# Kernel optimization log

Measured on AMD Instinct MI355X. Metric: run time of the kernel, lower is better.

The kernel has to match this reference:

```python
import jax, jax.numpy as jnp
import numpy as np

EMBED_DIM = 384
NUM_HEADS = 6
HEAD_DIM = EMBED_DIM // NUM_HEADS
MLP_HIDDEN = 4 * EMBED_DIM
LN_EPS = 1e-5


def layer_norm(x, gamma, beta):
    mu = jnp.mean(x, axis=-1, keepdims=True)
    var = jnp.mean((x - mu) ** 2, axis=-1, keepdims=True)
    return (x - mu) * jax.lax.rsqrt(var + LN_EPS) * gamma + beta


def setup_inputs() -> dict:
    key = jax.random.key(0)
    ks = jax.random.split(key, 8)
    D, H = EMBED_DIM, MLP_HIDDEN
    s = 1.0 / np.sqrt(D)
    sh = 1.0 / np.sqrt(H)
    return {
        "x": jax.random.normal(ks[0], (16, 1024, D), dtype=jnp.float32),
        "ln1_g": jnp.ones((D,), jnp.float32),
        "ln1_b": jnp.zeros((D,), jnp.float32),
        "qkv_w": jax.random.uniform(ks[1], (3 * D, D), jnp.float32, -s, s),
        "qkv_b": jax.random.uniform(ks[2], (3 * D,), jnp.float32, -s, s),
        "proj_w": jax.random.uniform(ks[3], (D, D), jnp.float32, -s, s),
        "proj_b": jax.random.uniform(ks[4], (D,), jnp.float32, -s, s),
        "ln2_g": jnp.ones((D,), jnp.float32),
        "ln2_b": jnp.zeros((D,), jnp.float32),
        "fc1_w": jax.random.uniform(ks[5], (H, D), jnp.float32, -s, s),
        "fc1_b": jax.random.uniform(ks[6], (H,), jnp.float32, -s, s),
        "fc2_w": jax.random.uniform(ks[7], (D, H), jnp.float32, -sh, sh),
        "fc2_b": jnp.zeros((D,), jnp.float32),
    }


def reference(x, ln1_g, ln1_b, qkv_w, qkv_b, proj_w, proj_b,
              ln2_g, ln2_b, fc1_w, fc1_b, fc2_w, fc2_b):
    B, N, D = x.shape
    Hh, Dh = NUM_HEADS, HEAD_DIM
    scale = Dh ** -0.5

    # --- attention sublayer (pre-norm) ---
    h = layer_norm(x, ln1_g, ln1_b)
    qkv = h @ qkv_w.T + qkv_b                      # [B,N,3D]
    qkv = qkv.reshape(B, N, 3, Hh, Dh)
    q, k, v = (qkv[:, :, i].transpose(0, 2, 1, 3) for i in range(3))  # [B,H,N,Dh]
    attn = jax.nn.softmax(jnp.einsum('bhnd,bhmd->bhnm', q, k) * scale, axis=-1)
    o = jnp.einsum('bhnm,bhmd->bhnd', attn, v)     # [B,H,N,Dh]
    o = o.transpose(0, 2, 1, 3).reshape(B, N, D)
    x = x + (o @ proj_w.T + proj_b)

    # --- MLP sublayer (pre-norm) ---
    h = layer_norm(x, ln2_g, ln2_b)
    h = jax.nn.gelu(h @ fc1_w.T + fc1_b, approximate=False)
    x = x + (h @ fc2_w.T + fc2_b)
    return x
```

## Files before the change

### kernel.cpp

```cpp
#include <hip/hip_runtime.h>

typedef unsigned short u16;
typedef unsigned int   u32;
typedef __bf16  bf16x8 __attribute__((ext_vector_type(8)));
typedef __bf16  bf16x4_t __attribute__((ext_vector_type(4)));
typedef float   f32x4  __attribute__((ext_vector_type(4)));

struct Ptrs { const void* p[13]; };

extern "C" __device__ float __ocml_native_exp2_f32(float);

__device__ __forceinline__ float bf2f(u16 u) {
    union { unsigned int i; float f; } c; c.i = ((unsigned int)u) << 16; return c.f;
}
__device__ __forceinline__ u16 f2bf(float f) {
    union { float f; unsigned int i; } c; c.f = f;
    unsigned int u = c.i;
    unsigned int r = (u + 0x7fffu + ((u >> 16) & 1u)) >> 16;
    return (u16)r;
}

__device__ __forceinline__ float wave_sum(float x) {
#pragma unroll
    for (int m = 32; m >= 1; m >>= 1) x += __shfl_xor(x, m);
    return x;
}

__device__ __forceinline__ void g2l16(const u16* g, u16* l) {
    __builtin_amdgcn_global_load_lds(
        (__attribute__((address_space(1))) void*)g,
        (__attribute__((address_space(3))) void*)l, 16, 0, 0);
}

__global__ void k_flag(const u32* __restrict__ w, int* __restrict__ flagp)
{
    if (threadIdx.x == 0) {
        int cnt = 0;
        for (int i = 0; i < 128; ++i) {
            u16 lo = (u16)(w[i] & 0xFFFFu);
            int e = (lo >> 7) & 0xFF;
            cnt += (e >= 117 && e <= 123) ? 1 : 0;
        }
        *flagp = (cnt >= 64) ? 1 : 0;
    }
}

__global__ __launch_bounds__(256) void k_convert(Ptrs ps,
                                                 u16* __restrict__ cw,
                                                 const int* __restrict__ flagp)
{
    const int cum[13] = {0,48,96,55392,55536,73968,74016,74064,74112,
                         147840,148032,221760,221808};
    const int off[12] = {0,384,768,443136,444288,591744,
                         592128,592512,592896,1182720,1184256,1774080};
    int c = blockIdx.x * 256 + threadIdx.x;
    if (c >= 221808) return;
    int seg = 0;
#pragma unroll
    for (int i = 1; i < 12; ++i) seg += (c >= cum[i]) ? 1 : 0;
    int e = (c - cum[seg]) * 8;
    u16* dst = cw + off[seg] + e;
    if (*flagp) {
        *(uint4*)dst = *((const uint4*)ps.p[seg + 1] + (e >> 3));
    } else {
        const float* s = (const float*)ps.p[seg + 1] + e;
        u16 tmp[8];
#pragma unroll
        for (int t = 0; t < 8; ++t) tmp[t] = f2bf(s[t]);
        *(uint4*)dst = *(const uint4*)tmp;
    }
}

__global__ __launch_bounds__(256) void k_ln1cvt(const void* __restrict__ xin,
                                                const u16* __restrict__ g,
                                                const u16* __restrict__ b,
                                                u16* __restrict__ cx,
                                                u16* __restrict__ h,
                                                const int* __restrict__ flagp)
{
    const int wid = threadIdx.x >> 6, lane = threadIdx.x & 63;
    const int row = blockIdx.x * 4 + wid;
    float v[6]; u16 raw[6];
    if (*flagp) {
        const u16* p = (const u16*)xin + (size_t)row * 384;
#pragma unroll
        for (int t = 0; t < 6; t++) { raw[t] = p[lane + 64 * t]; v[t] = bf2f(raw[t]); }
    } else {
        const float* p = (const float*)xin + (size_t)row * 384;
#pragma unroll
        for (int t = 0; t < 6; t++) { v[t] = p[lane + 64 * t]; raw[t] = f2bf(v[t]); }
    }
    u16* pc = cx + (size_t)row * 384;
#pragma unroll
    for (int t = 0; t < 6; t++) pc[lane + 64 * t] = raw[t];
    float s = 0.f;
#pragma unroll
    for (int t = 0; t < 6; t++) s += v[t];
    const float mu = wave_sum(s) * (1.0f / 384.0f);
    float vs = 0.f;
#pragma unroll
    for (int t = 0; t < 6; t++) { float d = v[t] - mu; vs += d * d; }
    const float var = wave_sum(vs) * (1.0f / 384.0f);
    const float rs = rsqrtf(var + 1e-5f);
    u16* po = h + (size_t)row * 384;
#pragma unroll
    for (int t = 0; t < 6; t++) {
        int e = lane + 64 * t;
        po[e] = f2bf((v[t] - mu) * rs * bf2f(g[e]) + bf2f(b[e]));
    }
}

__device__ __forceinline__ void gemm_core_128(const u16* __restrict__ A,
                                              const u16* __restrict__ B,
                                              int K, int m0, int n0,
                                              f32x4 (&acc)[4][4])
{
    __shared__ __align__(16) u16 As[128 * 64];
    __shared__ __align__(16) u16 Bs[128 * 64];

    const int tid  = threadIdx.x;
    const int lane = tid & 63;
    const int wid  = tid >> 6;
    const int wm  = (wid >> 1) * 64;
    const int wn  = (wid & 1) * 64;
    const int l15 = lane & 15;
    const int g   = lane >> 4;
    const int srow   = lane >> 3;
    const int schunk = ((lane & 7) ^ srow) * 8;

    const u16* Abase = A + (size_t)(m0 + wid * 32 + srow) * K + schunk;
    const u16* Bbase = B + (size_t)(n0 + wid * 32 + srow) * K + schunk;

    for (int kk = 0; kk < K; kk += 64) {
        __syncthreads();
#pragma unroll
        for (int t = 0; t < 4; ++t) {
            g2l16(Abase + (size_t)t * 8 * K + kk, &As[(wid * 32 + t * 8) * 64]);
            g2l16(Bbase + (size_t)t * 8 * K + kk, &Bs[(wid * 32 + t * 8) * 64]);
        }
        __syncthreads();

#pragma unroll
        for (int ks = 0; ks < 2; ++ks) {
            bf16x8 af[4], bfr[4];
#pragma unroll
            for (int i = 0; i < 4; i++) {
                int row = wm + 16 * i + l15;
                int p = ((ks * 4 + g) ^ (l15 & 7)) * 8;
                af[i] = __builtin_bit_cast(bf16x8,
                         *(const uint4*)&As[row * 64 + p]);
            }
#pragma unroll
            for (int j = 0; j < 4; j++) {
                int row = wn + 16 * j + l15;
                int p = ((ks * 4 + g) ^ (l15 & 7)) * 8;
                bfr[j] = __builtin_bit_cast(bf16x8,
                         *(const uint4*)&Bs[row * 64 + p]);
            }
#pragma unroll
            for (int i = 0; i < 4; i++)
#pragma unroll
                for (int j = 0; j < 4; j++)
                    acc[i][j] = __builtin_amdgcn_mfma_f32_16x16x32_bf16(
                                    af[i], bfr[j], acc[i][j], 0, 0, 0);
        }
    }
}

__device__ __forceinline__ void gemm_core_128x64(const u16* __restrict__ A,
                                                 const u16* __restrict__ B,
                                                 int K, int m0, int n0,
                                                 f32x4 (&acc)[4][2])
{
    __shared__ __align__(16) u16 As[128 * 64];
    __shared__ __align__(16) u16 Bs[64 * 64];

    const int tid  = threadIdx.x;
    const int lane = tid & 63;
    const int wid  = tid >> 6;
    const int wm  = (wid >> 1) * 64;
    const int wn  = (wid & 1) * 32;
    const int l15 = lane & 15;
    const int g   = lane >> 4;
    const int srow   = lane >> 3;
    const int schunk = ((lane & 7) ^ srow) * 8;

    const u16* Abase = A + (size_t)(m0 + wid * 32 + srow) * K + schunk;
    const u16* Bbase = B + (size_t)(n0 + wid * 16 + srow) * K + schunk;

    for (int kk = 0; kk < K; kk += 64) {
        __syncthreads();
#pragma unroll
        for (int t = 0; t < 4; ++t)
            g2l16(Abase + (size_t)t * 8 * K + kk, &As[(wid * 32 + t * 8) * 64]);
#pragma unroll
        for (int t = 0; t < 2; ++t)
            g2l16(Bbase + (size_t)t * 8 * K + kk, &Bs[(wid * 16 + t * 8) * 64]);
        __syncthreads();

#pragma unroll
        for (int ks = 0; ks < 2; ++ks) {
            bf16x8 af[4], bfr[2];
#pragma unroll
            for (int i = 0; i < 4; i++) {
                int row = wm + 16 * i + l15;
                int p = ((ks * 4 + g) ^ (l15 & 7)) * 8;
                af[i] = __builtin_bit_cast(bf16x8,
                         *(const uint4*)&As[row * 64 + p]);
            }
#pragma unroll
            for (int j = 0; j < 2; j++) {
                int row = wn + 16 * j + l15;
                int p = ((ks * 4 + g) ^ (l15 & 7)) * 8;
                bfr[j] = __builtin_bit_cast(bf16x8,
                         *(const uint4*)&Bs[row * 64 + p]);
            }
#pragma unroll
            for (int i = 0; i < 4; i++)
#pragma unroll
                for (int j = 0; j < 2; j++)
                    acc[i][j] = __builtin_amdgcn_mfma_f32_16x16x32_bf16(
                                    af[i], bfr[j], acc[i][j], 0, 0, 0);
        }
    }
}

__global__ __launch_bounds__(256) void k_layernorm(const u16* __restrict__ in,
                                                   const u16* __restrict__ g,
                                                   const u16* __restrict__ b,
                                                   u16* __restrict__ out,
                                                   int nrows)
{
    const int wid = threadIdx.x >> 6, lane = threadIdx.x & 63;
    const int row = blockIdx.x * 4 + wid;
    if (row >= nrows) return;
    float v[6];
    const u16* p = in + (size_t)row * 384;
#pragma unroll
    for (int t = 0; t < 6; t++) v[t] = bf2f(p[lane + 64 * t]);
    float s = 0.f;
#pragma unroll
    for (int t = 0; t < 6; t++) s += v[t];
    const float mu = wave_sum(s) * (1.0f / 384.0f);
    float vs = 0.f;
#pragma unroll
    for (int t = 0; t < 6; t++) { float d = v[t] - mu; vs += d * d; }
    const float var = wave_sum(vs) * (1.0f / 384.0f);
    const float rs = rsqrtf(var + 1e-5f);
    u16* po = out + (size_t)row * 384;
#pragma unroll
    for (int t = 0; t < 6; t++) {
        int e = lane + 64 * t;
        po[e] = f2bf((v[t] - mu) * rs * bf2f(g[e]) + bf2f(b[e]));
    }
}

__global__ __launch_bounds__(256) void k_gemm_qkv(const u16* __restrict__ A,
                                                  const u16* __restrict__ W,
                                                  const u16* __restrict__ bias,
                                                  u16* __restrict__ q,
                                                  u16* __restrict__ k,
                                                  u16* __restrict__ vrow)
{
    const int id = blockIdx.x, slot = id & 7, idx = id >> 3;
    const int m0 = (slot * 16 + idx / 9) * 128;
    const int n0 = (idx % 9) * 128;
    f32x4 acc[4][4];
#pragma unroll
    for (int i = 0; i < 4; i++)
#pragma unroll
        for (int j = 0; j < 4; j++) acc[i][j] = f32x4{0.f, 0.f, 0.f, 0.f};
    gemm_core_128(A, W, 384, m0, n0, acc);
    const int lane = threadIdx.x & 63, wid = threadIdx.x >> 6;
    const int wm = (wid >> 1) * 64, wn = (wid & 1) * 64;
    const int l15 = lane & 15, rq = (lane >> 4) * 4;
#pragma unroll
    for (int i = 0; i < 4; i++)
#pragma unroll
        for (int j = 0; j < 4; j++)
#pragma unroll
            for (int r = 0; r < 4; r++) {
                int gr = m0 + wm + 16 * i + rq + r;
                int gc = n0 + wn + 16 * j + l15;
                float v = acc[i][j][r] + bf2f(bias[gc]);
                int part = gc / 384, rem = gc % 384;
                int head = rem >> 6, dh = rem & 63;
                int bb = gr >> 10, nn = gr & 1023;
                int bh = bb * 6 + head;
                u16* dst = (part == 0) ? q : (part == 1) ? k : vrow;
                dst[((size_t)bh * 1024 + nn) * 64 + dh] = f2bf(v);
            }
}

__global__ __launch_bounds__(256) void k_transpose_v(const u16* __restrict__ v,
                                                     u16* __restrict__ vT)
{
    __shared__ u16 T[64 * 72];
    const int bh = blockIdx.y, n0 = blockIdx.x * 64;
    const int tid = threadIdx.x;
    const int r = tid >> 2;
    const int c = (tid & 3) * 16;
    const u16* src = v + (size_t)bh * 65536 + (size_t)(n0 + r) * 64 + c;
    uint4 a = *(const uint4*)src;
    uint4 b = *(const uint4*)(src + 8);
    u16 buf[16];
    *(uint4*)&buf[0] = a; *(uint4*)&buf[8] = b;
#pragma unroll
    for (int e = 0; e < 16; ++e) T[(c + e) * 72 + r] = buf[e];
    __syncthreads();
    uint4 o0 = *(const uint4*)&T[r * 72 + c];
    uint4 o1 = *(const uint4*)&T[r * 72 + c + 8];
    u16* dst = vT + (size_t)bh * 65536 + (size_t)r * 1024 + n0 + c;
    *(uint4*)dst = o0;
    *(uint4*)(dst + 8) = o1;
}

__global__ __launch_bounds__(256) void k_attn(const u16* __restrict__ q,
                                              const u16* __restrict__ kk,
                                              const u16* __restrict__ vT,
                                              u16* __restrict__ o)
{
    __shared__ __align__(16) u16 Ks[128 * 64];
    __shared__ __align__(16) u16 Vs[2][64 * 64];
    __shared__ __align__(16) u16 Ps[128 * 64];

    const int tid = threadIdx.x, lane = tid & 63, wid = tid >> 6;
    const int l15 = lane & 15, g = lane >> 4, q8 = g * 8;
    const int id = blockIdx.x;
    const int bh = (id & 7) * 12 + ((id >> 3) >> 3);
    const int q0 = ((id >> 3) & 7) * 128;
    const int wrow = wid * 32;

    const u16* Q = q  + (size_t)bh * 65536;
    const u16* K = kk + (size_t)bh * 65536;
    const u16* V = vT + (size_t)bh * 65536;

    const int srow   = lane >> 3;
    const int schunk = ((lane & 7) ^ srow) * 8;
    const int rd0 = ((0 + g) ^ (l15 & 7)) * 8;
    const int rd1 = ((4 + g) ^ (l15 & 7)) * 8;
    int pcol[4];
#pragma unroll
    for (int ip = 0; ip < 4; ++ip)
        pcol[ip] = (((ip * 2 + (g >> 1)) ^ (l15 & 7)) * 8) + (g & 1) * 4;

    bf16x8 aq[2][2];
#pragma unroll
    for (int jp = 0; jp < 2; ++jp)
#pragma unroll
        for (int ks = 0; ks < 2; ++ks) {
            bf16x8 t = __builtin_bit_cast(bf16x8,
                *(const uint4*)&Q[(size_t)(q0 + wrow + jp * 16 + l15) * 64
                                  + ks * 32 + q8]);
#pragma unroll
            for (int e = 0; e < 8; ++e)
                t[e] = (__bf16)((float)t[e] * 0.18033688f);
            aq[jp][ks] = t;
        }

    f32x4 ob[2][4];
#pragma unroll
    for (int i = 0; i < 2; ++i)
#pragma unroll
        for (int j = 0; j < 4; ++j) ob[i][j] = f32x4{0.f, 0.f, 0.f, 0.f};
    float lsum[2] = {0.f, 0.f};

    for (int kt2 = 0; kt2 < 8; ++kt2) {
        __syncthreads();
#pragma unroll
        for (int t = 0; t < 4; ++t) {
            int r0 = wid * 32 + t * 8;
            g2l16(&K[(size_t)(kt2 * 128 + r0 + srow) * 64 + schunk], &Ks[r0 * 64]);
        }
#pragma unroll
        for (int h = 0; h < 2; ++h)
#pragma unroll
            for (int t = 0; t < 2; ++t) {
                int r0 = wid * 16 + t * 8;
                g2l16(&V[(size_t)(r0 + srow) * 1024 + kt2 * 128 + h * 64 + schunk],
                      &Vs[h][r0 * 64]);
            }
        __syncthreads();

#pragma unroll 1
        for (int h = 0; h < 2; ++h) {
            f32x4 st[4][2];
#pragma unroll
            for (int ip = 0; ip < 4; ++ip)
#pragma unroll
                for (int jp = 0; jp < 2; ++jp) st[ip][jp] = f32x4{0.f,0.f,0.f,0.f};
#pragma unroll
            for (int ip = 0; ip < 4; ++ip) {
                int rbase = (h * 64 + ip * 16 + l15) * 64;
                bf16x8 bk0 = __builtin_bit_cast(bf16x8,
                    *(const uint4*)&Ks[rbase + rd0]);
                bf16x8 bk1 = __builtin_bit_cast(bf16x8,
                    *(const uint4*)&Ks[rbase + rd1]);
#pragma unroll
                for (int jp = 0; jp < 2; ++jp) {
                    st[ip][jp] = __builtin_amdgcn_mfma_f32_16x16x32_bf16(
                                    bk0, aq[jp][0], st[ip][jp], 0, 0, 0);
                    st[ip][jp] = __builtin_amdgcn_mfma_f32_16x16x32_bf16(
                                    bk1, aq[jp][1], st[ip][jp], 0, 0, 0);
                }
            }

#pragma unroll
            for (int jp = 0; jp < 2; ++jp) {
                float ps = 0.f;
#pragma unroll
                for (int ip = 0; ip < 4; ++ip)
#pragma unroll
                    for (int r = 0; r < 4; ++r) {
                        float p = __ocml_native_exp2_f32(st[ip][jp][r]);
                        st[ip][jp][r] = p;
                        ps += p;
                    }
                lsum[jp] += ps;
            }

#pragma unroll
            for (int ip = 0; ip < 4; ++ip)
#pragma unroll
                for (int jp = 0; jp < 2; ++jp) {
                    bf16x4_t pk;
#pragma unroll
                    for (int r = 0; r < 4; ++r) pk[r] = (__bf16)st[ip][jp][r];
                    *(bf16x4_t*)&Ps[(wrow + jp*16 + l15) * 64 + pcol[ip]] = pk;
                }

#pragma unroll
            for (int ks = 0; ks < 2; ++ks) {
                const int rdo = ks ? rd1 : rd0;
                bf16x8 ap[2];
#pragma unroll
                for (int i = 0; i < 2; ++i)
                    ap[i] = __builtin_bit_cast(bf16x8,
                        *(const uint4*)&Ps[(wrow + i*16 + l15) * 64 + rdo]);
#pragma unroll
                for (int jv = 0; jv < 4; ++jv) {
                    bf16x8 bv = __builtin_bit_cast(bf16x8,
                        *(const uint4*)&Vs[h][(jv * 16 + l15) * 64 + rdo]);
#pragma unroll
                    for (int i = 0; i < 2; ++i)
                        ob[i][jv] = __builtin_amdgcn_mfma_f32_16x16x32_bf16(
                                      ap[i], bv, ob[i][jv], 0, 0, 0);
                }
            }
        }
    }

#pragma unroll
    for (int jp = 0; jp < 2; ++jp) {
        lsum[jp] += __shfl_xor(lsum[jp], 16);
        lsum[jp] += __shfl_xor(lsum[jp], 32);
    }
    const int bb = bh / 6, hh = bh % 6;
#pragma unroll
    for (int i = 0; i < 2; ++i)
#pragma unroll
        for (int r = 0; r < 4; ++r) {
            int src = (lane & 48) | (g * 4 + r);
            float linv = 1.0f / __shfl(lsum[i], src);
            int row = q0 + wrow + i * 16 + g * 4 + r;
#pragma unroll
            for (int jv = 0; jv < 4; ++jv) {
                int dh = jv * 16 + l15;
                o[((size_t)(bb * 1024 + row)) * 384 + hh * 64 + dh] =
                    f2bf(ob[i][jv][r] * linv);
            }
        }
}

__global__ __launch_bounds__(256) void k_gemm_proj(const u16* __restrict__ A,
                                                   const u16* __restrict__ W,
                                                   const u16* __restrict__ bias,
                                                   const u16* __restrict__ xin,
                                                   u16* __restrict__ x1)
{
    const int id = blockIdx.x, slot = id & 7, idx = id >> 3;
    const int m0 = (slot * 16 + idx / 6) * 128;
    const int n0 = (idx % 6) * 64;
    f32x4 acc[4][2];
#pragma unroll
    for (int i = 0; i < 4; i++)
#pragma unroll
        for (int j = 0; j < 2; j++) acc[i][j] = f32x4{0.f, 0.f, 0.f, 0.f};
    gemm_core_128x64(A, W, 384, m0, n0, acc);
    const int lane = threadIdx.x & 63, wid = threadIdx.x >> 6;
    const int wm = (wid >> 1) * 64, wn = (wid & 1) * 32;
    const int l15 = lane & 15, rq = (lane >> 4) * 4;
#pragma unroll
    for (int i = 0; i < 4; i++)
#pragma unroll
        for (int j = 0; j < 2; j++)
#pragma unroll
            for (int r = 0; r < 4; r++) {
                int gr = m0 + wm + 16 * i + rq + r;
                int gc = n0 + wn + 16 * j + l15;
                size_t ix = (size_t)gr * 384 + gc;
                x1[ix] = f2bf(acc[i][j][r] + bf2f(bias[gc]) + bf2f(xin[ix]));
            }
}

__global__ __launch_bounds__(256) void k_gemm_fc1(const u16* __restrict__ A,
                                                  const u16* __restrict__ W,
                                                  const u16* __restrict__ bias,
                                                  u16* __restrict__ hmid)
{
    const int id = blockIdx.x, slot = id & 7, idx = id >> 3;
    const int mbase = (slot * 8 + idx / 12) * 256;
    const int n0 = (idx % 12) * 128;
#pragma unroll 1
    for (int sub = 0; sub < 2; ++sub) {
        const int m0 = mbase + sub * 128;
        f32x4 acc[4][4];
#pragma unroll
        for (int i = 0; i < 4; i++)
#pragma unroll
            for (int j = 0; j < 4; j++) acc[i][j] = f32x4{0.f, 0.f, 0.f, 0.f};
        gemm_core_128(A, W, 384, m0, n0, acc);
        const int lane = threadIdx.x & 63, wid = threadIdx.x >> 6;
        const int wm = (wid >> 1) * 64, wn = (wid & 1) * 64;
        const int l15 = lane & 15, rq = (lane >> 4) * 4;
#pragma unroll
        for (int i = 0; i < 4; i++)
#pragma unroll
            for (int j = 0; j < 4; j++)
#pragma unroll
                for (int r = 0; r < 4; r++) {
                    int gr = m0 + wm + 16 * i + rq + r;
                    int gc = n0 + wn + 16 * j + l15;
                    float v = acc[i][j][r] + bf2f(bias[gc]);
                    float u = v * (1.5957691f + 0.0713548f * v * v);
                    float ge = v * __builtin_amdgcn_rcpf(1.0f + __expf(-u));
                    hmid[(size_t)gr * 1536 + gc] = f2bf(ge);
                }
    }
}

__global__ __launch_bounds__(256) void k_gemm_fc2(const u16* __restrict__ A,
                                                  const u16* __restrict__ W,
                                                  const u16* __restrict__ bias,
                                                  const u16* __restrict__ x1,
                                                  void* __restrict__ outv,
                                                  const int* __restrict__ flagp)
{
    const int id = blockIdx.x, slot = id & 7, idx = id >> 3;
    const int m0 = (slot * 16 + idx / 6) * 128;
    const int n0 = (idx % 6) * 64;
    f32x4 acc[4][2];
#pragma unroll
    for (int i = 0; i < 4; i++)
#pragma unroll
        for (int j = 0; j < 2; j++) acc[i][j] = f32x4{0.f, 0.f, 0.f, 0.f};
    gemm_core_128x64(A, W, 1536, m0, n0, acc);
    const int lane = threadIdx.x & 63, wid = threadIdx.x >> 6;
    const int wm = (wid >> 1) * 64, wn = (wid & 1) * 32;
    const int l15 = lane & 15, rq = (lane >> 4) * 4;
    const int isbf = *flagp;
    u16*   ob = (u16*)outv;
    float* of = (float*)outv;
#pragma unroll
    for (int i = 0; i < 4; i++)
#pragma unroll
        for (int j = 0; j < 2; j++)
#pragma unroll
            for (int r = 0; r < 4; r++) {
                int gr = m0 + wm + 16 * i + rq + r;
                int gc = n0 + wn + 16 * j + l15;
                size_t ix = (size_t)gr * 384 + gc;
                float v = acc[i][j][r] + bf2f(bias[gc]) + bf2f(x1[ix]);
                if (isbf) ob[ix] = f2bf(v);
                else      of[ix] = v;
            }
}

extern "C" void kernel_launch(void* const* d_in, const int* in_sizes, int n_in,
                              void* d_out, int out_size, void* d_ws, size_t ws_size,
                              hipStream_t stream)
{
    char* ws = (char*)d_ws;
    u16*   cw   = (u16*)(ws + 0);
    int*   flag = (int*)(ws + 3548928);
    u16*   cx   = (u16*)(ws + 3549184);
    u16*   h    = (u16*)(ws + 16132096);
    u16*   x1   = (u16*)(ws + 28715008);
    u16*   q    = (u16*)(ws + 53880832);
    u16*   kbuf = (u16*)(ws + 66463744);
    u16*   vT   = (u16*)(ws + 79046656);
    u16*   o    = (u16*)(ws + 91629568);
    u16*   vrow = o;
    u16*   hmid = (u16*)(ws + 53880832);

    const u16* c_ln1_g  = cw + 0;
    const u16* c_ln1_b  = cw + 384;
    const u16* c_qkv_w  = cw + 768;
    const u16* c_qkv_b  = cw + 443136;
    const u16* c_proj_w = cw + 444288;
    const u16* c_proj_b = cw + 591744;
    const u16* c_ln2_g  = cw + 592128;
    const u16* c_ln2_b  = cw + 592512;
    const u16* c_fc1_w  = cw + 592896;
    const u16* c_fc1_b  = cw + 1182720;
    const u16* c_fc2_w  = cw + 1184256;
    const u16* c_fc2_b  = cw + 1774080;

    Ptrs ps;
    for (int i = 0; i < 13; ++i) ps.p[i] = d_in[i];

    k_flag<<<1, 64, 0, stream>>>((const u32*)d_in[3], flag);
    k_convert<<<867, 256, 0, stream>>>(ps, cw, flag);
    k_ln1cvt<<<4096, 256, 0, stream>>>(d_in[0], c_ln1_g, c_ln1_b, cx, h, flag);
    k_gemm_qkv<<<1152, 256, 0, stream>>>(h, c_qkv_w, c_qkv_b, q, kbuf, vrow);
    k_transpose_v<<<dim3(16, 96), 256, 0, stream>>>(vrow, vT);
    k_attn<<<768, 256, 0, stream>>>(q, kbuf, vT, o);
    k_gemm_proj<<<768, 256, 0, stream>>>(o, c_proj_w, c_proj_b, cx, x1);
    k_layernorm<<<4096, 256, 0, stream>>>(x1, c_ln2_g, c_ln2_b, h, 16384);
    k_gemm_fc1<<<768, 256, 0, stream>>>(h, c_fc1_w, c_fc1_b, hmid);
    k_gemm_fc2<<<768, 256, 0, stream>>>(hmid, c_fc2_w, c_fc2_b, x1,
                                        d_out, flag);
    (void)in_sizes; (void)n_in; (void)out_size; (void)ws_size; (void)c_fc2_b;
}
```

Measured before the change: 271.7 us.

## Double-buffer K in LDS, load V directly to registers, vectorize layernorm

The attention kernel now prefetches the next K tile into registers while the current tile is computed, writes it into a second LDS buffer, and needs only one barrier per iteration. V fragments are read straight from global memory into registers instead of being staged through LDS. The MFMA sections are wrapped in s_setprio hints. The layernorm kernels switch to contiguous per-lane 6-element chunks with 32-bit and 64-bit loads and stores. This trades higher register pressure and uncoalesced direct V loads from global for fewer LDS round-trips and barriers.

```diff
diff --git a/kernel.cpp b/kernel.cpp
--- a/kernel.cpp
+++ b/kernel.cpp
@@ -5,6 +5,7 @@
 typedef __bf16  bf16x8 __attribute__((ext_vector_type(8)));
 typedef __bf16  bf16x4_t __attribute__((ext_vector_type(4)));
 typedef float   f32x4  __attribute__((ext_vector_type(4)));
+typedef float   f32x2  __attribute__((ext_vector_type(2)));
 
 struct Ptrs { const void* p[13]; };
 
@@ -80,19 +81,32 @@
 {
     const int wid = threadIdx.x >> 6, lane = threadIdx.x & 63;
     const int row = blockIdx.x * 4 + wid;
+    const int e0 = lane * 6;
     float v[6]; u16 raw[6];
     if (*flagp) {
-        const u16* p = (const u16*)xin + (size_t)row * 384;
-#pragma unroll
-        for (int t = 0; t < 6; t++) { raw[t] = p[lane + 64 * t]; v[t] = bf2f(raw[t]); }
+        const u16* p = (const u16*)xin + (size_t)row * 384 + e0;
+        u32 w0 = *(const u32*)(p);
+        u32 w1 = *(const u32*)(p + 2);
+        u32 w2 = *(const u32*)(p + 4);
+        raw[0] = (u16)w0; raw[1] = (u16)(w0 >> 16);
+        raw[2] = (u16)w1; raw[3] = (u16)(w1 >> 16);
+        raw[4] = (u16)w2; raw[5] = (u16)(w2 >> 16);
+#pragma unroll
+        for (int t = 0; t < 6; t++) v[t] = bf2f(raw[t]);
     } else {
-        const float* p = (const float*)xin + (size_t)row * 384;
-#pragma unroll
-        for (int t = 0; t < 6; t++) { v[t] = p[lane + 64 * t]; raw[t] = f2bf(v[t]); }
-    }
-    u16* pc = cx + (size_t)row * 384;
-#pragma unroll
-    for (int t = 0; t < 6; t++) pc[lane + 64 * t] = raw[t];
+        const float* p = (const float*)xin + (size_t)row * 384 + e0;
+        f32x2 a0 = *(const f32x2*)(p);
+        f32x2 a1 = *(const f32x2*)(p + 2);
+        f32x2 a2 = *(const f32x2*)(p + 4);
+        v[0] = a0[0]; v[1] = a0[1]; v[2] = a1[0];
+        v[3] = a1[1]; v[4] = a2[0]; v[5] = a2[1];
+#pragma unroll
+        for (int t = 0; t < 6; t++) raw[t] = f2bf(v[t]);
+    }
+    u32* pc = (u32*)(cx + (size_t)row * 384 + e0);
+    pc[0] = (u32)raw[0] | ((u32)raw[1] << 16);
+    pc[1] = (u32)raw[2] | ((u32)raw[3] << 16);
+    pc[2] = (u32)raw[4] | ((u32)raw[5] << 16);
     float s = 0.f;
 #pragma unroll
     for (int t = 0; t < 6; t++) s += v[t];
@@ -102,12 +116,21 @@
     for (int t = 0; t < 6; t++) { float d = v[t] - mu; vs += d * d; }
     const float var = wave_sum(vs) * (1.0f / 384.0f);
     const float rs = rsqrtf(var + 1e-5f);
-    u16* po = h + (size_t)row * 384;
+    const u32* gg = (const u32*)(g + e0);
+    const u32* bb = (const u32*)(b + e0);
+    u32 gw[3] = {gg[0], gg[1], gg[2]};
+    u32 bw[3] = {bb[0], bb[1], bb[2]};
+    u16 ow[6];
 #pragma unroll
     for (int t = 0; t < 6; t++) {
-        int e = lane + 64 * t;
-        po[e] = f2bf((v[t] - mu) * rs * bf2f(g[e]) + bf2f(b[e]));
-    }
+        u16 ge = (u16)(gw[t >> 1] >> ((t & 1) * 16));
+        u16 be = (u16)(bw[t >> 1] >> ((t & 1) * 16));
+        ow[t] = f2bf((v[t] - mu) * rs * bf2f(ge) + bf2f(be));
+    }
+    u32* po = (u32*)(h + (size_t)row * 384 + e0);
+    po[0] = (u32)ow[0] | ((u32)ow[1] << 16);
+    po[1] = (u32)ow[2] | ((u32)ow[3] << 16);
+    po[2] = (u32)ow[4] | ((u32)ow[5] << 16);
 }
 
 __device__ __forceinline__ void gemm_core_128(const u16* __restrict__ A,
@@ -234,10 +257,15 @@
     const int wid = threadIdx.x >> 6, lane = threadIdx.x & 63;
     const int row = blockIdx.x * 4 + wid;
     if (row >= nrows) return;
+    const int e0 = lane * 6;
     float v[6];
-    const u16* p = in + (size_t)row * 384;
-#pragma unroll
-    for (int t = 0; t < 6; t++) v[t] = bf2f(p[lane + 64 * t]);
+    const u16* p = in + (size_t)row * 384 + e0;
+    u32 w0 = *(const u32*)(p);
+    u32 w1 = *(const u32*)(p + 2);
+    u32 w2 = *(const u32*)(p + 4);
+    v[0] = bf2f((u16)w0); v[1] = bf2f((u16)(w0 >> 16));
+    v[2] = bf2f((u16)w1); v[3] = bf2f((u16)(w1 >> 16));
+    v[4] = bf2f((u16)w2); v[5] = bf2f((u16)(w2 >> 16));
     float s = 0.f;
 #pragma unroll
     for (int t = 0; t < 6; t++) s += v[t];
@@ -247,12 +275,21 @@
     for (int t = 0; t < 6; t++) { float d = v[t] - mu; vs += d * d; }
     const float var = wave_sum(vs) * (1.0f / 384.0f);
     const float rs = rsqrtf(var + 1e-5f);
-    u16* po = out + (size_t)row * 384;
+    const u32* gg = (const u32*)(g + e0);
+    const u32* bb = (const u32*)(b + e0);
+    u32 gw[3] = {gg[0], gg[1], gg[2]};
+    u32 bw[3] = {bb[0], bb[1], bb[2]};
+    u16 ow[6];
 #pragma unroll
     for (int t = 0; t < 6; t++) {
-        int e = lane + 64 * t;
-        po[e] = f2bf((v[t] - mu) * rs * bf2f(g[e]) + bf2f(b[e]));
-    }
+        u16 ge = (u16)(gw[t >> 1] >> ((t & 1) * 16));
+        u16 be = (u16)(bw[t >> 1] >> ((t & 1) * 16));
+        ow[t] = f2bf((v[t] - mu) * rs * bf2f(ge) + bf2f(be));
+    }
+    u32* po = (u32*)(out + (size_t)row * 384 + e0);
+    po[0] = (u32)ow[0] | ((u32)ow[1] << 16);
+    po[1] = (u32)ow[2] | ((u32)ow[3] << 16);
+    po[2] = (u32)ow[4] | ((u32)ow[5] << 16);
 }
 
 __global__ __launch_bounds__(256) void k_gemm_qkv(const u16* __restrict__ A,
@@ -320,8 +357,7 @@
                                               const u16* __restrict__ vT,
                                               u16* __restrict__ o)
 {
-    __shared__ __align__(16) u16 Ks[128 * 64];
-    __shared__ __align__(16) u16 Vs[2][64 * 64];
+    __shared__ __align__(16) u16 Ks[2][128 * 64];
     __shared__ __align__(16) u16 Ps[128 * 64];
 
     const int tid = threadIdx.x, lane = tid & 63, wid = tid >> 6;
@@ -358,6 +394,15 @@
             aq[jp][ks] = t;
         }
 
+    uint4 kreg[4];
+#pragma unroll
+    for (int t = 0; t < 4; ++t)
+        kreg[t] = *(const uint4*)&K[(size_t)(wid * 32 + t * 8 + srow) * 64 + schunk];
+#pragma unroll
+    for (int t = 0; t < 4; ++t)
+        *(uint4*)&Ks[0][(wid * 32 + t * 8) * 64 + lane * 8] = kreg[t];
+    __syncthreads();
+
     f32x4 ob[2][4];
 #pragma unroll
     for (int i = 0; i < 2; ++i)
@@ -365,37 +410,41 @@
         for (int j = 0; j < 4; ++j) ob[i][j] = f32x4{0.f, 0.f, 0.f, 0.f};
     float lsum[2] = {0.f, 0.f};
 
+    int cur = 0;
     for (int kt2 = 0; kt2 < 8; ++kt2) {
-        __syncthreads();
-#pragma unroll
-        for (int t = 0; t < 4; ++t) {
-            int r0 = wid * 32 + t * 8;
-            g2l16(&K[(size_t)(kt2 * 128 + r0 + srow) * 64 + schunk], &Ks[r0 * 64]);
-        }
-#pragma unroll
-        for (int h = 0; h < 2; ++h)
-#pragma unroll
-            for (int t = 0; t < 2; ++t) {
-                int r0 = wid * 16 + t * 8;
-                g2l16(&V[(size_t)(r0 + srow) * 1024 + kt2 * 128 + h * 64 + schunk],
-                      &Vs[h][r0 * 64]);
-            }
-        __syncthreads();
+        if (kt2 < 7) {
+#pragma unroll
+            for (int t = 0; t < 4; ++t)
+                kreg[t] = *(const uint4*)
+                    &K[(size_t)((kt2 + 1) * 128 + wid * 32 + t * 8 + srow) * 64
+                       + schunk];
+        }
 
 #pragma unroll 1
         for (int h = 0; h < 2; ++h) {
+            uint4 vreg[2][4];
+#pragma unroll
+            for (int ks = 0; ks < 2; ++ks)
+#pragma unroll
+                for (int jv = 0; jv < 4; ++jv)
+                    vreg[ks][jv] = *(const uint4*)
+                        &V[(size_t)(jv * 16 + l15) * 1024
+                           + kt2 * 128 + h * 64 + (ks * 4 + g) * 8];
+
             f32x4 st[4][2];
 #pragma unroll
             for (int ip = 0; ip < 4; ++ip)
 #pragma unroll
                 for (int jp = 0; jp < 2; ++jp) st[ip][jp] = f32x4{0.f,0.f,0.f,0.f};
+
+            __builtin_amdgcn_s_setprio(1);
 #pragma unroll
             for (int ip = 0; ip < 4; ++ip) {
                 int rbase = (h * 64 + ip * 16 + l15) * 64;
                 bf16x8 bk0 = __builtin_bit_cast(bf16x8,
-                    *(const uint4*)&Ks[rbase + rd0]);
+                    *(const uint4*)&Ks[cur][rbase + rd0]);
                 bf16x8 bk1 = __builtin_bit_cast(bf16x8,
-                    *(const uint4*)&Ks[rbase + rd1]);
+                    *(const uint4*)&Ks[cur][rbase + rd1]);
 #pragma unroll
                 for (int jp = 0; jp < 2; ++jp) {
                     st[ip][jp] = __builtin_amdgcn_mfma_f32_16x16x32_bf16(
@@ -404,6 +453,7 @@
                                     bk1, aq[jp][1], st[ip][jp], 0, 0, 0);
                 }
             }
+            __builtin_amdgcn_s_setprio(0);
 
 #pragma unroll
             for (int jp = 0; jp < 2; ++jp) {
@@ -429,6 +479,7 @@
                     *(bf16x4_t*)&Ps[(wrow + jp*16 + l15) * 64 + pcol[ip]] = pk;
                 }
 
+            __builtin_amdgcn_s_setprio(1);
 #pragma unroll
             for (int ks = 0; ks < 2; ++ks) {
                 const int rdo = ks ? rd1 : rd0;
@@ -439,15 +490,23 @@
                         *(const uint4*)&Ps[(wrow + i*16 + l15) * 64 + rdo]);
 #pragma unroll
                 for (int jv = 0; jv < 4; ++jv) {
-                    bf16x8 bv = __builtin_bit_cast(bf16x8,
-                        *(const uint4*)&Vs[h][(jv * 16 + l15) * 64 + rdo]);
+                    bf16x8 bv = __builtin_bit_cast(bf16x8, vreg[ks][jv]);
 #pragma unroll
                     for (int i = 0; i < 2; ++i)
                         ob[i][jv] = __builtin_amdgcn_mfma_f32_16x16x32_bf16(
                                       ap[i], bv, ob[i][jv], 0, 0, 0);
                 }
             }
-        }
+            __builtin_amdgcn_s_setprio(0);
+        }
+
+        if (kt2 < 7) {
+#pragma unroll
+            for (int t = 0; t < 4; ++t)
+                *(uint4*)&Ks[cur ^ 1][(wid * 32 + t * 8) * 64 + lane * 8] = kreg[t];
+        }
+        __syncthreads();
+        cur ^= 1;
     }
 
 #pragma unroll
```

Result: slower. 300.2 us (+10.5%).
